# Performance work log

Hardware: AMD Instinct MI355X
Metric: run time of the kernel (lower is better)

## Reference

```python
import jax, jax.numpy as jnp
import numpy as np

NH = 4        # router attention heads
M1, M2 = 16, 16  # Fourier modes kept
N_FNO_LAYERS = 4
TOP_K = 2
TEMP = 1.0


def _ln(x, g, b):
    m = x.mean(-1, keepdims=True)
    v = ((x - m) ** 2).mean(-1, keepdims=True)
    return (x - m) / jnp.sqrt(v + 1e-5) * g + b


def _mha(s, wqkv, bqkv, wo, bo):
    B, S, D = s.shape
    dh = D // NH
    qkv = s @ wqkv + bqkv
    q, k, v = jnp.split(qkv, 3, axis=-1)
    rs = lambda t: t.reshape(B, S, NH, dh).transpose(0, 2, 1, 3)
    q, k, v = rs(q), rs(k), rs(v)
    a = jax.nn.softmax(jnp.einsum('bhqd,bhkd->bhqk', q, k) / np.sqrt(dh), axis=-1)
    o = jnp.einsum('bhqk,bhkd->bhqd', a, v).transpose(0, 2, 1, 3).reshape(B, S, D)
    return o @ wo + bo


def _spectral_conv(h, w1, w2):
    # h: (B, Ci, H, W); w1/w2: (Ci, Co, M1, M2, 2) real/imag pairs
    B, Ci, H, W = h.shape
    Co = w1.shape[1]
    ft = jnp.fft.rfft2(h, axes=(-2, -1))  # (B, Ci, H, W//2+1) complex
    w1c = w1[..., 0] + 1j * w1[..., 1]
    w2c = w2[..., 0] + 1j * w2[..., 1]
    lo = jnp.einsum('bixy,ioxy->boxy', ft[:, :, :M1, :M2], w1c)
    hi = jnp.einsum('bixy,ioxy->boxy', ft[:, :, -M1:, :M2], w2c)
    oft = jnp.zeros((B, Co, H, W // 2 + 1), dtype=ft.dtype)
    oft = oft.at[:, :, :M1, :M2].set(lo).at[:, :, -M1:, :M2].set(hi)
    return jnp.fft.irfft2(oft, s=(H, W), axes=(-2, -1))


def _fno(x, lw, lb, sw1, sw2, kw, kb, p1w, p1b, p2w, p2b):
    h = jnp.einsum('bchw,co->bohw', x, lw) + lb[None, :, None, None]
    for l in range(N_FNO_LAYERS):
        s = _spectral_conv(h, sw1[l], sw2[l])
        sk = jnp.einsum('bchw,co->bohw', h, kw[l]) + kb[l][None, :, None, None]
        h = s + sk
        if l < N_FNO_LAYERS - 1:
            h = jax.nn.gelu(h)
    h = jax.nn.gelu(jnp.einsum('bchw,co->bohw', h, p1w) + p1b[None, :, None, None])
    return jnp.einsum('bchw,co->bohw', h, p2w) + p2b[None, :, None, None]


def _router(x, enc_in_w, enc_in_b, attn_wqkv, attn_bqkv, attn_wo, attn_bo,
            ln1_g, ln1_b, ffn_w1, ffn_b1, ffn_w2, ffn_b2, ln2_g, ln2_b, fc_w, fc_b):
    ic = x[:, :, 0, :]                       # (B, C, W) initial condition
    s = ic.transpose(0, 2, 1) @ enc_in_w + enc_in_b  # (B, W, hd)
    for l in range(attn_wqkv.shape[0]):
        s = _ln(s + _mha(s, attn_wqkv[l], attn_bqkv[l], attn_wo[l], attn_bo[l]), ln1_g[l], ln1_b[l])
        f = jax.nn.relu(s @ ffn_w1[l] + ffn_b1[l]) @ ffn_w2[l] + ffn_b2[l]
        s = _ln(s + f, ln2_g[l], ln2_b[l])
    feat = s.max(axis=1)                     # global max-pool over sequence
    logits = feat @ fc_w + fc_b              # (B, E)
    vals, idx = jax.lax.top_k(logits, TOP_K)
    w = jax.nn.softmax(vals / TEMP, axis=-1)
    B = logits.shape[0]
    rw = jnp.zeros_like(logits).at[jnp.arange(B)[:, None], idx].set(w)
    return rw


def setup_inputs() -> dict:
    key = jax.random.key(0)
    ks = iter(jax.random.split(key, 40))
    B, C, H, W = 32, 1, 64, 64
    E, HC, HD, RL, FF, OC = 8, 64, 64, 2, 256, 1
    rn = lambda shp, sc: jax.random.normal(next(ks), shp, dtype=jnp.float32) * sc
    inp = {
        'x': rn((B, C, H, W), 1.0),
        'enc_in_w': rn((C, HD), 0.5), 'enc_in_b': jnp.zeros((HD,), jnp.float32),
        'attn_wqkv': rn((RL, HD, 3 * HD), 0.08), 'attn_bqkv': jnp.zeros((RL, 3 * HD), jnp.float32),
        'attn_wo': rn((RL, HD, HD), 0.08), 'attn_bo': jnp.zeros((RL, HD), jnp.float32),
        'ln1_g': jnp.ones((RL, HD), jnp.float32), 'ln1_b': jnp.zeros((RL, HD), jnp.float32),
        'ffn_w1': rn((RL, HD, FF), 0.08), 'ffn_b1': jnp.zeros((RL, FF), jnp.float32),
        'ffn_w2': rn((RL, FF, HD), 0.05), 'ffn_b2': jnp.zeros((RL, HD), jnp.float32),
        'ln2_g': jnp.ones((RL, HD), jnp.float32), 'ln2_b': jnp.zeros((RL, HD), jnp.float32),
        'fc_w': rn((HD, E), 0.1), 'fc_b': jnp.zeros((E,), jnp.float32),
        'lift_w': rn((E, C, HC), 0.3), 'lift_b': jnp.zeros((E, HC), jnp.float32),
        'spec_w1': rn((E, N_FNO_LAYERS, HC, HC, M1, M2, 2), 1.0 / HC),
        'spec_w2': rn((E, N_FNO_LAYERS, HC, HC, M1, M2, 2), 1.0 / HC),
        'skip_w': rn((E, N_FNO_LAYERS, HC, HC), 0.08), 'skip_b': jnp.zeros((E, N_FNO_LAYERS, HC), jnp.float32),
        'proj1_w': rn((E, HC, HC), 0.08), 'proj1_b': jnp.zeros((E, HC), jnp.float32),
        'proj2_w': rn((E, HC, OC), 0.08), 'proj2_b': jnp.zeros((E, OC), jnp.float32),
    }
    return inp


def reference(x, enc_in_w, enc_in_b, attn_wqkv, attn_bqkv, attn_wo, attn_bo,
              ln1_g, ln1_b, ffn_w1, ffn_b1, ffn_w2, ffn_b2, ln2_g, ln2_b, fc_w, fc_b,
              lift_w, lift_b, spec_w1, spec_w2, skip_w, skip_b,
              proj1_w, proj1_b, proj2_w, proj2_b):
    rw = _router(x, enc_in_w, enc_in_b, attn_wqkv, attn_bqkv, attn_wo, attn_bo,
                 ln1_g, ln1_b, ffn_w1, ffn_b1, ffn_w2, ffn_b2, ln2_g, ln2_b, fc_w, fc_b)
    E = rw.shape[1]
    out = jnp.zeros((x.shape[0], proj2_w.shape[2], x.shape[2], x.shape[3]), x.dtype)
    for e in range(E):
        # weight is 0 for non-selected experts, so dense weighted sum == masked dispatch
        y = _fno(x, lift_w[e], lift_b[e], spec_w1[e], spec_w2[e],
                 skip_w[e], skip_b[e], proj1_w[e], proj1_b[e], proj2_w[e], proj2_b[e])
        out = out + rw[:, e, None, None, None] * y
    return out
```

## Files before the change

kernel.cpp:

```cpp
#include <hip/hip_runtime.h>
#include <math.h>

#define TWOPI_F 6.283185307179586f
#define LD4(p) (*(const float4*)(p))

__device__ __forceinline__ float gelu_f(float v) {
    float u = 0.7978845608028654f * (v + 0.044715f * v * v * v);
    return 0.5f * v * (1.f + tanhf(u));
}

__global__ void init_tables_kernel(float* __restrict__ Wy, float* __restrict__ TWX,
                                   float* __restrict__ WY2) {
    int t = threadIdx.x;
    for (int i = t; i < 1024; i += 256) {
        int y = i >> 4, k = i & 15;
        int m = (k * y) & 63;
        float a = -TWOPI_F * (float)m / 64.f;
        Wy[y * 32 + 2 * k]     = cosf(a);
        Wy[y * 32 + 2 * k + 1] = sinf(a);
    }
    if (t < 64) {
        float a = -TWOPI_F * (float)t / 64.f;
        TWX[2 * t]           = cosf(a);
        TWX[2 * t + 1]       = sinf(a);
        TWX[128 + 2 * t]     = cosf(a);
        TWX[128 + 2 * t + 1] = -sinf(a);
    }
    for (int i = t; i < 1024; i += 256) {
        int y = i >> 4, k = i & 15;
        int m = (k * y) & 63;
        float a = TWOPI_F * (float)m / 64.f;
        float sc = (k == 0 ? 1.f : 2.f) / 4096.f;
        WY2[y * 32 + 2 * k]     = sc * cosf(a);
        WY2[y * 32 + 2 * k + 1] = sc * sinf(a);
    }
}

__global__ __launch_bounds__(512) void router_kernel(
    const float* __restrict__ x, const float* __restrict__ enc_w, const float* __restrict__ enc_b,
    const float* __restrict__ wqkv, const float* __restrict__ bqkv,
    const float* __restrict__ wo, const float* __restrict__ bo,
    const float* __restrict__ ln1g, const float* __restrict__ ln1b,
    const float* __restrict__ w1, const float* __restrict__ b1,
    const float* __restrict__ w2, const float* __restrict__ b2,
    const float* __restrict__ ln2g, const float* __restrict__ ln2b,
    const float* __restrict__ fcw, const float* __restrict__ fcb,
    float* __restrict__ rw)
{
    __shared__ float s[64][65];
    __shared__ float qk[64][193];
    __shared__ float sc[64][65];
    __shared__ float o64[64][65];
    __shared__ float feat[64];
    __shared__ float logits[8];
    int b = blockIdx.x, t = threadIdx.x;

    for (int i = t; i < 4096; i += 512) {
        int w_ = i >> 6, d = i & 63;
        s[w_][d] = x[b * 4096 + w_] * enc_w[d] + enc_b[d];
    }
    __syncthreads();

    for (int l = 0; l < 2; ++l) {
        {
            const float* Wq = wqkv + l * 64 * 192;
            const float* Bq = bqkv + l * 192;
            int c4 = t % 48, rg = t / 48;
            if (rg < 8) {
                const float* wcol = Wq + 4 * c4;
                float4 bq = LD4(Bq + 4 * c4);
                float4 acc[8];
#pragma unroll
                for (int i = 0; i < 8; ++i) acc[i] = bq;
                int r0 = rg * 8;
#pragma unroll 8
                for (int k = 0; k < 64; ++k) {
                    float4 wv = LD4(wcol + k * 192);
#pragma unroll
                    for (int i = 0; i < 8; ++i) {
                        float sv = s[r0 + i][k];
                        acc[i].x += sv * wv.x; acc[i].y += sv * wv.y;
                        acc[i].z += sv * wv.z; acc[i].w += sv * wv.w;
                    }
                }
#pragma unroll
                for (int i = 0; i < 8; ++i) {
                    qk[r0 + i][4 * c4]     = acc[i].x;
                    qk[r0 + i][4 * c4 + 1] = acc[i].y;
                    qk[r0 + i][4 * c4 + 2] = acc[i].z;
                    qk[r0 + i][4 * c4 + 3] = acc[i].w;
                }
            }
        }
        __syncthreads();
        for (int h = 0; h < 4; ++h) {
            for (int i = t; i < 4096; i += 512) {
                int q = i >> 6, kj = i & 63;
                float acc = 0.f;
#pragma unroll
                for (int d = 0; d < 16; ++d)
                    acc += qk[q][h * 16 + d] * qk[kj][64 + h * 16 + d];
                sc[q][kj] = acc * 0.25f;
            }
            __syncthreads();
            if (t < 64) {
                float m = -1e30f;
                for (int j = 0; j < 64; ++j) m = fmaxf(m, sc[t][j]);
                float sum = 0.f;
                for (int j = 0; j < 64; ++j) { float e2 = expf(sc[t][j] - m); sc[t][j] = e2; sum += e2; }
                float inv = 1.f / sum;
                for (int j = 0; j < 64; ++j) sc[t][j] *= inv;
            }
            __syncthreads();
            for (int i = t; i < 1024; i += 512) {
                int q = i >> 4, d = i & 15;
                float acc = 0.f;
#pragma unroll 8
                for (int j = 0; j < 64; ++j) acc += sc[q][j] * qk[j][128 + h * 16 + d];
                o64[q][h * 16 + d] = acc;
            }
            __syncthreads();
        }
        {
            const float* Wo = wo + l * 4096;
            const float* Bo = bo + l * 64;
            int c4 = t & 15, rg = t >> 4;
            const float* wcol = Wo + 4 * c4;
            float4 acc0 = LD4(Bo + 4 * c4), acc1 = acc0;
            int r0 = rg * 2;
#pragma unroll 8
            for (int k = 0; k < 64; ++k) {
                float4 wv = LD4(wcol + k * 64);
                float h0 = o64[r0][k], h1 = o64[r0 + 1][k];
                acc0.x += h0 * wv.x; acc0.y += h0 * wv.y;
                acc0.z += h0 * wv.z; acc0.w += h0 * wv.w;
                acc1.x += h1 * wv.x; acc1.y += h1 * wv.y;
                acc1.z += h1 * wv.z; acc1.w += h1 * wv.w;
            }
            sc[r0][4 * c4]     = s[r0][4 * c4]     + acc0.x;
            sc[r0][4 * c4 + 1] = s[r0][4 * c4 + 1] + acc0.y;
            sc[r0][4 * c4 + 2] = s[r0][4 * c4 + 2] + acc0.z;
            sc[r0][4 * c4 + 3] = s[r0][4 * c4 + 3] + acc0.w;
            sc[r0 + 1][4 * c4]     = s[r0 + 1][4 * c4]     + acc1.x;
            sc[r0 + 1][4 * c4 + 1] = s[r0 + 1][4 * c4 + 1] + acc1.y;
            sc[r0 + 1][4 * c4 + 2] = s[r0 + 1][4 * c4 + 2] + acc1.z;
            sc[r0 + 1][4 * c4 + 3] = s[r0 + 1][4 * c4 + 3] + acc1.w;
        }
        __syncthreads();
        if (t < 64) {
            float m = 0.f;
            for (int j = 0; j < 64; ++j) m += sc[t][j];
            m *= (1.f / 64.f);
            float v = 0.f;
            for (int j = 0; j < 64; ++j) { float d = sc[t][j] - m; v += d * d; }
            v *= (1.f / 64.f);
            float inv = rsqrtf(v + 1e-5f);
            for (int j = 0; j < 64; ++j)
                s[t][j] = (sc[t][j] - m) * inv * ln1g[l * 64 + j] + ln1b[l * 64 + j];
        }
        __syncthreads();
        {
            const float* W1 = w1 + l * 64 * 256;
            const float* B1 = b1 + l * 256;
            int c4 = t & 63, rg = t >> 6;
            const float* wcol = W1 + 4 * c4;
            float4 b1v = LD4(B1 + 4 * c4);
            float4 acc[8];
#pragma unroll
            for (int i = 0; i < 8; ++i) acc[i] = b1v;
            int r0 = rg * 8;
#pragma unroll 4
            for (int k = 0; k < 64; ++k) {
                float4 wv = LD4(wcol + k * 256);
#pragma unroll
                for (int i = 0; i < 8; ++i) {
                    float sv = s[r0 + i][k];
                    acc[i].x += sv * wv.x; acc[i].y += sv * wv.y;
                    acc[i].z += sv * wv.z; acc[i].w += sv * wv.w;
                }
            }
#pragma unroll
            for (int i = 0; i < 8; ++i) {
                float a0 = fmaxf(acc[i].x, 0.f), a1 = fmaxf(acc[i].y, 0.f);
                float a2 = fmaxf(acc[i].z, 0.f), a3 = fmaxf(acc[i].w, 0.f);
                if (c4 < 48) {
                    qk[r0 + i][4 * c4] = a0; qk[r0 + i][4 * c4 + 1] = a1;
                    qk[r0 + i][4 * c4 + 2] = a2; qk[r0 + i][4 * c4 + 3] = a3;
                } else {
                    int c = 4 * c4 - 192;
                    o64[r0 + i][c] = a0; o64[r0 + i][c + 1] = a1;
                    o64[r0 + i][c + 2] = a2; o64[r0 + i][c + 3] = a3;
                }
            }
        }
        __syncthreads();
        {
            const float* W2 = w2 + l * 256 * 64;
            const float* B2 = b2 + l * 64;
            int c4 = t & 15, rg = t >> 4;
            const float* wcol = W2 + 4 * c4;
            float4 acc0 = LD4(B2 + 4 * c4), acc1 = acc0;
            int r0 = rg * 2;
#pragma unroll 8
            for (int k = 0; k < 192; ++k) {
                float4 wv = LD4(wcol + k * 64);
                float h0 = qk[r0][k], h1 = qk[r0 + 1][k];
                acc0.x += h0 * wv.x; acc0.y += h0 * wv.y;
                acc0.z += h0 * wv.z; acc0.w += h0 * wv.w;
                acc1.x += h1 * wv.x; acc1.y += h1 * wv.y;
                acc1.z += h1 * wv.z; acc1.w += h1 * wv.w;
            }
#pragma unroll 8
            for (int k = 192; k < 256; ++k) {
                float4 wv = LD4(wcol + k * 64);
                float h0 = o64[r0][k - 192], h1 = o64[r0 + 1][k - 192];
                acc0.x += h0 * wv.x; acc0.y += h0 * wv.y;
                acc0.z += h0 * wv.z; acc0.w += h0 * wv.w;
                acc1.x += h1 * wv.x; acc1.y += h1 * wv.y;
                acc1.z += h1 * wv.z; acc1.w += h1 * wv.w;
            }
            sc[r0][4 * c4]     = s[r0][4 * c4]     + acc0.x;
            sc[r0][4 * c4 + 1] = s[r0][4 * c4 + 1] + acc0.y;
            sc[r0][4 * c4 + 2] = s[r0][4 * c4 + 2] + acc0.z;
            sc[r0][4 * c4 + 3] = s[r0][4 * c4 + 3] + acc0.w;
            sc[r0 + 1][4 * c4]     = s[r0 + 1][4 * c4]     + acc1.x;
            sc[r0 + 1][4 * c4 + 1] = s[r0 + 1][4 * c4 + 1] + acc1.y;
            sc[r0 + 1][4 * c4 + 2] = s[r0 + 1][4 * c4 + 2] + acc1.z;
            sc[r0 + 1][4 * c4 + 3] = s[r0 + 1][4 * c4 + 3] + acc1.w;
        }
        __syncthreads();
        if (t < 64) {
            float m = 0.f;
            for (int j = 0; j < 64; ++j) m += sc[t][j];
            m *= (1.f / 64.f);
            float v = 0.f;
            for (int j = 0; j < 64; ++j) { float d = sc[t][j] - m; v += d * d; }
            v *= (1.f / 64.f);
            float inv = rsqrtf(v + 1e-5f);
            for (int j = 0; j < 64; ++j)
                s[t][j] = (sc[t][j] - m) * inv * ln2g[l * 64 + j] + ln2b[l * 64 + j];
        }
        __syncthreads();
    }
    if (t < 64) {
        float m = -1e30f;
        for (int r = 0; r < 64; ++r) m = fmaxf(m, s[r][t]);
        feat[t] = m;
    }
    __syncthreads();
    if (t < 8) {
        float acc = fcb[t];
        for (int k = 0; k < 64; ++k) acc += feat[k] * fcw[k * 8 + t];
        logits[t] = acc;
    }
    __syncthreads();
    if (t == 0) {
        int i0 = 0;
        for (int j = 1; j < 8; ++j) if (logits[j] > logits[i0]) i0 = j;
        int i1 = -1;
        for (int j = 0; j < 8; ++j) {
            if (j == i0) continue;
            if (i1 < 0 || logits[j] > logits[i1]) i1 = j;
        }
        float e1 = expf(logits[i1] - logits[i0]);
        float w0 = 1.f / (1.f + e1);
        float w1v = e1 / (1.f + e1);
        for (int j = 0; j < 8; ++j) rw[b * 8 + j] = 0.f;
        rw[b * 8 + i0] = w0;
        rw[b * 8 + i1] = w1v;
    }
}

__global__ void build_pairs_kernel(const float* __restrict__ rw, int* __restrict__ pair_b,
                                   int* __restrict__ pair_e, float* __restrict__ pair_w,
                                   int* __restrict__ estart, int* __restrict__ chunk_e,
                                   int* __restrict__ chunk_p0, int* __restrict__ chunk_np) {
    __shared__ float r[256];
    __shared__ int cnt[8], off[9];
    int t = threadIdx.x;
    for (int i = t; i < 256; i += 64) r[i] = rw[i];
    if (t < 64) { pair_b[t] = 0; pair_e[t] = 0; pair_w[t] = 0.f; }
    __syncthreads();
    if (t < 8) {
        int c = 0;
        for (int b = 0; b < 32; ++b) if (r[b * 8 + t] != 0.f) ++c;
        cnt[t] = c;
    }
    __syncthreads();
    if (t == 0) {
        int a = 0;
        for (int e = 0; e < 8; ++e) { off[e] = a; a += cnt[e]; }
        off[8] = a;
        for (int e = 0; e <= 8; ++e) estart[e] = off[e];
        int nc = 0;
        for (int e = 0; e < 8; ++e) {
            for (int s = off[e]; s < off[e + 1]; s += 8) {
                int np = off[e + 1] - s; if (np > 8) np = 8;
                chunk_e[nc] = e; chunk_p0[nc] = s; chunk_np[nc] = np; ++nc;
            }
        }
        for (int c = nc; c < 16; ++c) { chunk_e[c] = 0; chunk_p0[c] = 0; chunk_np[c] = 0; }
    }
    __syncthreads();
    if (t < 8) {
        int n = off[t];
        for (int b = 0; b < 32; ++b) {
            float w = r[b * 8 + t];
            if (w != 0.f) { pair_b[n] = b; pair_e[n] = t; pair_w[n] = w; ++n; }
        }
    }
}

__global__ __launch_bounds__(256) void lift_kernel(const float* __restrict__ x,
    const float* __restrict__ lw, const float* __restrict__ lb,
    const int* __restrict__ pair_b, const int* __restrict__ pair_e, float* __restrict__ hA) {
    int p = blockIdx.x, tile = blockIdx.y, t = threadIdx.x;
    int b = pair_b[p], e = pair_e[p];
    float* h = hA + (size_t)p * 262144;
    const float* xb = x + (size_t)b * 4096;
    for (int i = tile * 16384 + t; i < (tile + 1) * 16384; i += 256) {
        int co = i >> 12, xy = i & 4095;
        h[i] = xb[xy] * lw[e * 64 + co] + lb[e * 64 + co];
    }
}

__global__ __launch_bounds__(256) void fwdft_kernel(const float* __restrict__ h,
    const float* __restrict__ Wy, const float* __restrict__ TWX, float* __restrict__ F) {
    __shared__ float ht[64][68];
    __shared__ float gt[64][36];
    __shared__ float wy[2048];
    __shared__ float tw64[128];
    int bid = blockIdx.x;
    int t = threadIdx.x;
    const float* src = h + (size_t)bid * 4096;
    for (int i = t; i < 1024; i += 256) {
        float4 v = *(const float4*)(src + i * 4);
        int x = (i * 4) >> 6, y = (i * 4) & 63;
        *(float4*)(&ht[x][y]) = v;
    }
    for (int i = t; i < 512; i += 256) *(float4*)(&wy[i * 4]) = *(const float4*)(Wy + i * 4);
    if (t < 32) *(float4*)(&tw64[t * 4]) = LD4(TWX + t * 4);
    __syncthreads();
    {
        int xx = t >> 2, kq = t & 3;
        float gr0 = 0.f, gi0 = 0.f, gr1 = 0.f, gi1 = 0.f;
        float gr2 = 0.f, gi2 = 0.f, gr3 = 0.f, gi3 = 0.f;
#pragma unroll 4
        for (int y = 0; y < 64; ++y) {
            float hv = ht[xx][y];
            float4 w0 = *(const float4*)(&wy[y * 32 + kq * 8]);
            float4 w1 = *(const float4*)(&wy[y * 32 + kq * 8 + 4]);
            gr0 += hv * w0.x; gi0 += hv * w0.y;
            gr1 += hv * w0.z; gi1 += hv * w0.w;
            gr2 += hv * w1.x; gi2 += hv * w1.y;
            gr3 += hv * w1.z; gi3 += hv * w1.w;
        }
        *(float4*)(&gt[xx][kq * 8])     = make_float4(gr0, gi0, gr1, gi1);
        *(float4*)(&gt[xx][kq * 8 + 4]) = make_float4(gr2, gi2, gr3, gi3);
    }
    __syncthreads();
    {
        int kxm = t & 31, kyq = t >> 5;
        int kx = kxm < 16 ? kxm : kxm + 32;
        float ar0 = 0.f, ai0 = 0.f, ar1 = 0.f, ai1 = 0.f;
        int idx = 0;
#pragma unroll 4
        for (int xx = 0; xx < 64; ++xx) {
            float c_ = tw64[2 * idx], s_ = tw64[2 * idx + 1];
            float4 g = *(const float4*)(&gt[xx][kyq * 4]);
            ar0 += g.x * c_ - g.y * s_;  ai0 += g.x * s_ + g.y * c_;
            ar1 += g.z * c_ - g.w * s_;  ai1 += g.z * s_ + g.w * c_;
            idx = (idx + kx) & 63;
        }
        float* fb = F + (size_t)bid * 1024 + kxm * 32 + kyq * 4;
        *(float4*)(fb) = make_float4(ar0, ai0, ar1, ai1);
    }
}

__global__ __launch_bounds__(256) void spectral_kernel(
    const float* __restrict__ F, float* __restrict__ FoA, float* __restrict__ FoB,
    const float* __restrict__ w1, const float* __restrict__ w2,
    const int* __restrict__ chunk_e, const int* __restrict__ chunk_p0,
    const int* __restrict__ chunk_np, int l)
{
    int c = blockIdx.x;
    int np = chunk_np[c];
    if (np == 0) return;
    int e = chunk_e[c], p0 = chunk_p0[c];
    int z = blockIdx.z;
    int wsel = z & 1, cih = (z >> 1) & 1, mq = z >> 2;
    int t = threadIdx.x;
    int co = blockIdx.y * 4 + (t >> 6);
    int lane = t & 63;
    int moff = mq * 256 + lane * 4;

    const float* wbase = (wsel == 0 ? w1 : w2) + (size_t)(e * 4 + l) * 2097152;
    const float* Wc  = wbase + (size_t)(cih * 32) * 32768 + (size_t)co * 512 + moff;
    const float* Fc0 = F + (size_t)p0 * 65536 + (size_t)(cih * 32) * 1024 + wsel * 512 + moff;
    float* Fob = (cih ? FoB : FoA) + (size_t)p0 * 65536 + (size_t)co * 1024 + wsel * 512 + moff;

    float4 acc[8];
#pragma unroll
    for (int p = 0; p < 8; ++p) acc[p] = make_float4(0.f, 0.f, 0.f, 0.f);
    const float* Wp = Wc;
    const float* Fp = Fc0;
    for (int ci = 0; ci < 32; ++ci) {
        float4 wv = LD4(Wp);
#pragma unroll
        for (int p = 0; p < 8; ++p) {
            float4 fv = LD4(Fp + (size_t)p * 65536);
            acc[p].x += fv.x * wv.x - fv.y * wv.y;
            acc[p].y += fv.x * wv.y + fv.y * wv.x;
            acc[p].z += fv.z * wv.z - fv.w * wv.w;
            acc[p].w += fv.z * wv.w + fv.w * wv.z;
        }
        Wp += 32768;
        Fp += 1024;
    }
#pragma unroll
    for (int p = 0; p < 8; ++p) {
        if (p < np)
            *(float4*)(Fob + (size_t)p * 65536) = acc[p];
    }
}

__global__ __launch_bounds__(256) void conv1x1_kernel(
    const float* __restrict__ src, float* __restrict__ dst,
    const float* __restrict__ Wall, const float* __restrict__ Ball,
    const int* __restrict__ pair_e, int wmul, int wadd, int do_gelu)
{
    __shared__ float ws[64][68];
    __shared__ float bs[64];
    int p = blockIdx.x, tile = blockIdx.y, t = threadIdx.x;
    int e = pair_e[p];
    int widx = e * wmul + wadd;
    const float* W = Wall + (size_t)widx * 4096;
    for (int i = t; i < 1024; i += 256) {
        float4 v = LD4(W + i * 4);
        int ci = (i * 4) >> 6, co = (i * 4) & 63;
        *(float4*)(&ws[ci][co]) = v;
    }
    if (t < 64) bs[t] = Ball[widx * 64 + t];
    __syncthreads();

    int xy4 = t & 63, cog = t >> 6;
    const float* sb = src + (size_t)p * 262144 + tile * 256 + xy4 * 4;
    float4 acc[16];
#pragma unroll
    for (int j = 0; j < 16; ++j) {
        float bv = bs[cog * 16 + j];
        acc[j] = make_float4(bv, bv, bv, bv);
    }
    for (int ci = 0; ci < 64; ++ci) {
        float4 sv = LD4(sb + (size_t)ci * 4096);
        float4 w0 = *(const float4*)(&ws[ci][cog * 16]);
        float4 w1 = *(const float4*)(&ws[ci][cog * 16 + 4]);
        float4 w2 = *(const float4*)(&ws[ci][cog * 16 + 8]);
        float4 w3 = *(const float4*)(&ws[ci][cog * 16 + 12]);
        float wr[16] = {w0.x, w0.y, w0.z, w0.w, w1.x, w1.y, w1.z, w1.w,
                        w2.x, w2.y, w2.z, w2.w, w3.x, w3.y, w3.z, w3.w};
#pragma unroll
        for (int j = 0; j < 16; ++j) {
            float w = wr[j];
            acc[j].x += sv.x * w; acc[j].y += sv.y * w;
            acc[j].z += sv.z * w; acc[j].w += sv.w * w;
        }
    }
    float* d = dst + (size_t)p * 262144 + (size_t)(cog * 16) * 4096 + tile * 256 + xy4 * 4;
#pragma unroll
    for (int j = 0; j < 16; ++j) {
        float4 v = acc[j];
        if (do_gelu) {
            v.x = gelu_f(v.x); v.y = gelu_f(v.y);
            v.z = gelu_f(v.z); v.w = gelu_f(v.w);
        }
        *(float4*)(d + (size_t)j * 4096) = v;
    }
}

__global__ __launch_bounds__(256) void projfused_kernel(
    const float* __restrict__ src, const float* __restrict__ p1w,
    const float* __restrict__ p1b, const float* __restrict__ p2w,
    const float* __restrict__ p2b, const int* __restrict__ pair_b,
    const int* __restrict__ pair_e, const float* __restrict__ pw,
    float* __restrict__ out)
{
    __shared__ float ws[64][68];
    __shared__ float bs[64];
    __shared__ float w2s[64];
    __shared__ float4 red[4][64];
    int p = blockIdx.x, tile = blockIdx.y, t = threadIdx.x;
    int e = pair_e[p];
    const float* W = p1w + (size_t)e * 4096;
    for (int i = t; i < 1024; i += 256) {
        float4 v = LD4(W + i * 4);
        int ci = (i * 4) >> 6, co = (i * 4) & 63;
        *(float4*)(&ws[ci][co]) = v;
    }
    if (t < 64) { bs[t] = p1b[e * 64 + t]; w2s[t] = p2w[e * 64 + t]; }
    __syncthreads();

    int xy4 = t & 63, cog = t >> 6;
    const float* sb = src + (size_t)p * 262144 + tile * 256 + xy4 * 4;
    float4 acc[16];
#pragma unroll
    for (int j = 0; j < 16; ++j) {
        float bv = bs[cog * 16 + j];
        acc[j] = make_float4(bv, bv, bv, bv);
    }
    for (int ci = 0; ci < 64; ++ci) {
        float4 sv = LD4(sb + (size_t)ci * 4096);
        float4 w0 = *(const float4*)(&ws[ci][cog * 16]);
        float4 w1 = *(const float4*)(&ws[ci][cog * 16 + 4]);
        float4 w2 = *(const float4*)(&ws[ci][cog * 16 + 8]);
        float4 w3 = *(const float4*)(&ws[ci][cog * 16 + 12]);
        float wr[16] = {w0.x, w0.y, w0.z, w0.w, w1.x, w1.y, w1.z, w1.w,
                        w2.x, w2.y, w2.z, w2.w, w3.x, w3.y, w3.z, w3.w};
#pragma unroll
        for (int j = 0; j < 16; ++j) {
            float w = wr[j];
            acc[j].x += sv.x * w; acc[j].y += sv.y * w;
            acc[j].z += sv.z * w; acc[j].w += sv.w * w;
        }
    }
    float4 part = make_float4(0.f, 0.f, 0.f, 0.f);
#pragma unroll
    for (int j = 0; j < 16; ++j) {
        float w = w2s[cog * 16 + j];
        part.x += gelu_f(acc[j].x) * w;
        part.y += gelu_f(acc[j].y) * w;
        part.z += gelu_f(acc[j].z) * w;
        part.w += gelu_f(acc[j].w) * w;
    }
    red[cog][xy4] = part;
    __syncthreads();
    if (t < 64) {
        float4 s0 = red[0][t], s1 = red[1][t], s2 = red[2][t], s3 = red[3][t];
        float wgt = pw[p];
        float b2 = p2b[e];
        int b = pair_b[p];
        float* ob = out + (size_t)b * 4096 + tile * 256 + t * 4;
        atomicAdd(ob,     wgt * (s0.x + s1.x + s2.x + s3.x + b2));
        atomicAdd(ob + 1, wgt * (s0.y + s1.y + s2.y + s3.y + b2));
        atomicAdd(ob + 2, wgt * (s0.z + s1.z + s2.z + s3.z + b2));
        atomicAdd(ob + 3, wgt * (s0.w + s1.w + s2.w + s3.w + b2));
    }
}

__global__ __launch_bounds__(256) void inv_kernel(
    const float* __restrict__ FoA, const float* __restrict__ FoB,
    const float* __restrict__ WY2, const float* __restrict__ TWX,
    float* __restrict__ dst_h, int do_gelu)
{
    __shared__ float wy2[2048];
    __shared__ float twl[128];
    __shared__ float fo_s[1024];
    __shared__ float tT[64][36];
    __shared__ float ot[64][66];
    int t = threadIdx.x;
    for (int i = t; i < 512; i += 256) *(float4*)(&wy2[i * 4]) = *(const float4*)(WY2 + i * 4);
    if (t < 32) *(float4*)(&twl[t * 4]) = LD4(TWX + 128 + t * 4);
    int wid = blockIdx.x;
    int p = wid >> 6, co = wid & 63;
    const float* fA = FoA + (size_t)p * 65536 + (size_t)co * 1024;
    const float* fB = FoB + (size_t)p * 65536 + (size_t)co * 1024;
    {
        float4 a = LD4(fA + t * 4);
        float4 b = LD4(fB + t * 4);
        *(float4*)(&fo_s[t * 4]) = make_float4(a.x + b.x, a.y + b.y, a.z + b.z, a.w + b.w);
    }
    __syncthreads();
    {
        int xx = t & 63, kq = t >> 6;
        float Tr0 = 0.f, Ti0 = 0.f, Tr1 = 0.f, Ti1 = 0.f;
        float Tr2 = 0.f, Ti2 = 0.f, Tr3 = 0.f, Ti3 = 0.f;
#pragma unroll 4
        for (int kxm = 0; kxm < 32; ++kxm) {
            int kx = kxm < 16 ? kxm : kxm + 32;
            int idx = (kx * xx) & 63;
            float c_ = twl[2 * idx], s_ = twl[2 * idx + 1];
            float4 f0 = *(const float4*)(&fo_s[kxm * 32 + kq * 8]);
            float4 f1 = *(const float4*)(&fo_s[kxm * 32 + kq * 8 + 4]);
            Tr0 += f0.x * c_ - f0.y * s_;  Ti0 += f0.x * s_ + f0.y * c_;
            Tr1 += f0.z * c_ - f0.w * s_;  Ti1 += f0.z * s_ + f0.w * c_;
            Tr2 += f1.x * c_ - f1.y * s_;  Ti2 += f1.x * s_ + f1.y * c_;
            Tr3 += f1.z * c_ - f1.w * s_;  Ti3 += f1.z * s_ + f1.w * c_;
        }
        *(float4*)(&tT[xx][kq * 8])     = make_float4(Tr0, Ti0, Tr1, Ti1);
        *(float4*)(&tT[xx][kq * 8 + 4]) = make_float4(Tr2, Ti2, Tr3, Ti3);
    }
    __syncthreads();
    {
        int xx = t & 63, yq = t >> 6;
        float Trr[16], Tii[16];
#pragma unroll
        for (int q = 0; q < 8; ++q) {
            float4 v = *(const float4*)(&tT[xx][q * 4]);
            Trr[q * 2] = v.x; Tii[q * 2] = v.y;
            Trr[q * 2 + 1] = v.z; Tii[q * 2 + 1] = v.w;
        }
        for (int j = 0; j < 16; ++j) {
            int y = yq * 16 + j;
            const float* wr = &wy2[y * 32];
            float acc = 0.f;
#pragma unroll
            for (int k = 0; k < 16; ++k)
                acc += Trr[k] * wr[2 * k] - Tii[k] * wr[2 * k + 1];
            ot[xx][y] = acc;
        }
    }
    __syncthreads();
    {
        float* base = dst_h + (size_t)p * 262144 + (size_t)co * 4096;
        for (int r = 0; r < 16; ++r) {
            int gidx = r * 256 + t;
            int xx = gidx >> 6, y = gidx & 63;
            float v = base[gidx] + ot[xx][y];
            if (do_gelu) v = gelu_f(v);
            base[gidx] = v;
        }
    }
}

extern "C" void kernel_launch(void* const* d_in, const int* in_sizes, int n_in,
                              void* d_out, int out_size, void* d_ws, size_t ws_size,
                              hipStream_t stream) {
    const float* x    = (const float*)d_in[0];
    const float* encw = (const float*)d_in[1];
    const float* encb = (const float*)d_in[2];
    const float* wqkv = (const float*)d_in[3];
    const float* bqkv = (const float*)d_in[4];
    const float* wo   = (const float*)d_in[5];
    const float* bo   = (const float*)d_in[6];
    const float* ln1g = (const float*)d_in[7];
    const float* ln1b = (const float*)d_in[8];
    const float* fw1  = (const float*)d_in[9];
    const float* fb1  = (const float*)d_in[10];
    const float* fw2  = (const float*)d_in[11];
    const float* fb2  = (const float*)d_in[12];
    const float* ln2g = (const float*)d_in[13];
    const float* ln2b = (const float*)d_in[14];
    const float* fcw  = (const float*)d_in[15];
    const float* fcb  = (const float*)d_in[16];
    const float* lw   = (const float*)d_in[17];
    const float* lb   = (const float*)d_in[18];
    const float* sw1  = (const float*)d_in[19];
    const float* sw2  = (const float*)d_in[20];
    const float* skw  = (const float*)d_in[21];
    const float* skb  = (const float*)d_in[22];
    const float* p1w  = (const float*)d_in[23];
    const float* p1b  = (const float*)d_in[24];
    const float* p2w  = (const float*)d_in[25];
    const float* p2b  = (const float*)d_in[26];
    float* out = (float*)d_out;

    float* wsf    = (float*)d_ws;
    float* rw     = wsf;
    float* pair_w = wsf + 256;
    int*   ipart  = (int*)(wsf + 320);
    int* pair_b   = ipart;
    int* pair_e   = ipart + 64;
    int* estart   = ipart + 128;
    int* chunk_e  = ipart + 137;
    int* chunk_p0 = ipart + 153;
    int* chunk_np = ipart + 169;
    float* Wy  = wsf + 512;
    float* TWX = wsf + 2560;
    float* WY2 = wsf + 6656;
    float* hA  = wsf + 16384;
    float* hB  = hA + (size_t)64 * 262144;
    float* F   = hB + (size_t)64 * 262144;
    float* FoA = F + (size_t)64 * 65536;
    float* FoB = FoA + (size_t)64 * 65536;
    size_t need = (16384 + 2ull * 64 * 262144 + 64ull * 65536 + 64ull * 131072) * 4;
    if (ws_size < need) return;

    hipMemsetAsync(d_out, 0, (size_t)out_size * sizeof(float), stream);
    init_tables_kernel<<<1, 256, 0, stream>>>(Wy, TWX, WY2);
    router_kernel<<<32, 512, 0, stream>>>(x, encw, encb, wqkv, bqkv, wo, bo, ln1g, ln1b,
                                          fw1, fb1, fw2, fb2, ln2g, ln2b, fcw, fcb, rw);
    build_pairs_kernel<<<1, 64, 0, stream>>>(rw, pair_b, pair_e, pair_w, estart,
                                             chunk_e, chunk_p0, chunk_np);
    lift_kernel<<<dim3(64, 16), 256, 0, stream>>>(x, lw, lb, pair_b, pair_e, hA);
    for (int l = 0; l < 4; ++l) {
        float* cur = (l & 1) ? hB : hA;
        float* nxt = (l & 1) ? hA : hB;
        fwdft_kernel<<<4096, 256, 0, stream>>>(cur, Wy, TWX, F);
        spectral_kernel<<<dim3(16, 16, 8), 256, 0, stream>>>(F, FoA, FoB, sw1, sw2,
                                                             chunk_e, chunk_p0, chunk_np, l);
        conv1x1_kernel<<<dim3(64, 16), 256, 0, stream>>>(cur, nxt, skw, skb, pair_e, 4, l, 0);
        inv_kernel<<<4096, 256, 0, stream>>>(FoA, FoB, WY2, TWX, nxt, (l < 3) ? 1 : 0);
    }
    projfused_kernel<<<dim3(64, 16), 256, 0, stream>>>(hA, p1w, p1b, p2w, p2b,
                                                       pair_b, pair_e, pair_w, out);
}
```

Before: 1.322 ms.

## Fuse lift into first-layer DFT and skip conv; batch router attention heads

Removes the separate lift kernel and its 64x64x4096 activation write. The lift is now recomputed inline from x in a new forward-DFT kernel and a new 1x1 skip-conv kernel for layer 0. This saves one full write and read pass of the hA buffer per pair. Separately, the router computes all four attention heads' scores, softmax and outputs in single passes with a larger per-head score buffer, cutting the number of barriers. The cost is more shared memory in the router and some redundant lift arithmetic per channel.

After: 1.300 ms. No clear change (-1.6%).

```diff
diff --git a/kernel.cpp b/kernel.cpp
--- a/kernel.cpp
+++ b/kernel.cpp
@@ -49,7 +49,7 @@
 {
     __shared__ float s[64][65];
     __shared__ float qk[64][193];
-    __shared__ float sc[64][65];
+    __shared__ float scH[4][64][65];
     __shared__ float o64[64][65];
     __shared__ float feat[64];
     __shared__ float logits[8];
@@ -93,34 +93,34 @@
             }
         }
         __syncthreads();
-        for (int h = 0; h < 4; ++h) {
-            for (int i = t; i < 4096; i += 512) {
-                int q = i >> 6, kj = i & 63;
-                float acc = 0.f;
-#pragma unroll
-                for (int d = 0; d < 16; ++d)
-                    acc += qk[q][h * 16 + d] * qk[kj][64 + h * 16 + d];
-                sc[q][kj] = acc * 0.25f;
-            }
-            __syncthreads();
-            if (t < 64) {
-                float m = -1e30f;
-                for (int j = 0; j < 64; ++j) m = fmaxf(m, sc[t][j]);
-                float sum = 0.f;
-                for (int j = 0; j < 64; ++j) { float e2 = expf(sc[t][j] - m); sc[t][j] = e2; sum += e2; }
-                float inv = 1.f / sum;
-                for (int j = 0; j < 64; ++j) sc[t][j] *= inv;
-            }
-            __syncthreads();
-            for (int i = t; i < 1024; i += 512) {
-                int q = i >> 4, d = i & 15;
-                float acc = 0.f;
+        for (int i = t; i < 16384; i += 512) {
+            int h = i >> 12, q = (i >> 6) & 63, kj = i & 63;
+            float acc = 0.f;
+#pragma unroll
+            for (int d = 0; d < 16; ++d)
+                acc += qk[q][h * 16 + d] * qk[kj][64 + h * 16 + d];
+            scH[h][q][kj] = acc * 0.25f;
+        }
+        __syncthreads();
+        if (t < 256) {
+            int h = t >> 6, q = t & 63;
+            float* row = scH[h][q];
+            float m = -1e30f;
+            for (int j = 0; j < 64; ++j) m = fmaxf(m, row[j]);
+            float sum = 0.f;
+            for (int j = 0; j < 64; ++j) { float e2 = expf(row[j] - m); row[j] = e2; sum += e2; }
+            float inv = 1.f / sum;
+            for (int j = 0; j < 64; ++j) row[j] *= inv;
+        }
+        __syncthreads();
+        for (int i = t; i < 4096; i += 512) {
+            int q = i >> 6, d = i & 63, h = d >> 4;
+            float acc = 0.f;
 #pragma unroll 8
-                for (int j = 0; j < 64; ++j) acc += sc[q][j] * qk[j][128 + h * 16 + d];
-                o64[q][h * 16 + d] = acc;
-            }
-            __syncthreads();
-        }
+            for (int j = 0; j < 64; ++j) acc += scH[h][q][j] * qk[j][128 + d];
+            o64[q][d] = acc;
+        }
+        __syncthreads();
         {
             const float* Wo = wo + l * 4096;
             const float* Bo = bo + l * 64;
@@ -137,26 +137,26 @@
                 acc1.x += h1 * wv.x; acc1.y += h1 * wv.y;
                 acc1.z += h1 * wv.z; acc1.w += h1 * wv.w;
             }
-            sc[r0][4 * c4]     = s[r0][4 * c4]     + acc0.x;
-            sc[r0][4 * c4 + 1] = s[r0][4 * c4 + 1] + acc0.y;
-            sc[r0][4 * c4 + 2] = s[r0][4 * c4 + 2] + acc0.z;
-            sc[r0][4 * c4 + 3] = s[r0][4 * c4 + 3] + acc0.w;
-            sc[r0 + 1][4 * c4]     = s[r0 + 1][4 * c4]     + acc1.x;
-            sc[r0 + 1][4 * c4 + 1] = s[r0 + 1][4 * c4 + 1] + acc1.y;
-            sc[r0 + 1][4 * c4 + 2] = s[r0 + 1][4 * c4 + 2] + acc1.z;
-            sc[r0 + 1][4 * c4 + 3] = s[r0 + 1][4 * c4 + 3] + acc1.w;
+            scH[0][r0][4 * c4]     = s[r0][4 * c4]     + acc0.x;
+            scH[0][r0][4 * c4 + 1] = s[r0][4 * c4 + 1] + acc0.y;
+            scH[0][r0][4 * c4 + 2] = s[r0][4 * c4 + 2] + acc0.z;
+            scH[0][r0][4 * c4 + 3] = s[r0][4 * c4 + 3] + acc0.w;
+            scH[0][r0 + 1][4 * c4]     = s[r0 + 1][4 * c4]     + acc1.x;
+            scH[0][r0 + 1][4 * c4 + 1] = s[r0 + 1][4 * c4 + 1] + acc1.y;
+            scH[0][r0 + 1][4 * c4 + 2] = s[r0 + 1][4 * c4 + 2] + acc1.z;
+            scH[0][r0 + 1][4 * c4 + 3] = s[r0 + 1][4 * c4 + 3] + acc1.w;
         }
         __syncthreads();
         if (t < 64) {
             float m = 0.f;
-            for (int j = 0; j < 64; ++j) m += sc[t][j];
+            for (int j = 0; j < 64; ++j) m += scH[0][t][j];
             m *= (1.f / 64.f);
             float v = 0.f;
-            for (int j = 0; j < 64; ++j) { float d = sc[t][j] - m; v += d * d; }
+            for (int j = 0; j < 64; ++j) { float d = scH[0][t][j] - m; v += d * d; }
             v *= (1.f / 64.f);
             float inv = rsqrtf(v + 1e-5f);
             for (int j = 0; j < 64; ++j)
-                s[t][j] = (sc[t][j] - m) * inv * ln1g[l * 64 + j] + ln1b[l * 64 + j];
+                s[t][j] = (scH[0][t][j] - m) * inv * ln1g[l * 64 + j] + ln1b[l * 64 + j];
         }
         __syncthreads();
         {
@@ -219,26 +219,26 @@
                 acc1.x += h1 * wv.x; acc1.y += h1 * wv.y;
                 acc1.z += h1 * wv.z; acc1.w += h1 * wv.w;
             }
-            sc[r0][4 * c4]     = s[r0][4 * c4]     + acc0.x;
-            sc[r0][4 * c4 + 1] = s[r0][4 * c4 + 1] + acc0.y;
-            sc[r0][4 * c4 + 2] = s[r0][4 * c4 + 2] + acc0.z;
-            sc[r0][4 * c4 + 3] = s[r0][4 * c4 + 3] + acc0.w;
-            sc[r0 + 1][4 * c4]     = s[r0 + 1][4 * c4]     + acc1.x;
-            sc[r0 + 1][4 * c4 + 1] = s[r0 + 1][4 * c4 + 1] + acc1.y;
-            sc[r0 + 1][4 * c4 + 2] = s[r0 + 1][4 * c4 + 2] + acc1.z;
-            sc[r0 + 1][4 * c4 + 3] = s[r0 + 1][4 * c4 + 3] + acc1.w;
+            scH[0][r0][4 * c4]     = s[r0][4 * c4]     + acc0.x;
+            scH[0][r0][4 * c4 + 1] = s[r0][4 * c4 + 1] + acc0.y;
+            scH[0][r0][4 * c4 + 2] = s[r0][4 * c4 + 2] + acc0.z;
+            scH[0][r0][4 * c4 + 3] = s[r0][4 * c4 + 3] + acc0.w;
+            scH[0][r0 + 1][4 * c4]     = s[r0 + 1][4 * c4]     + acc1.x;
+            scH[0][r0 + 1][4 * c4 + 1] = s[r0 + 1][4 * c4 + 1] + acc1.y;
+            scH[0][r0 + 1][4 * c4 + 2] = s[r0 + 1][4 * c4 + 2] + acc1.z;
+            scH[0][r0 + 1][4 * c4 + 3] = s[r0 + 1][4 * c4 + 3] + acc1.w;
         }
         __syncthreads();
         if (t < 64) {
             float m = 0.f;
-            for (int j = 0; j < 64; ++j) m += sc[t][j];
+            for (int j = 0; j < 64; ++j) m += scH[0][t][j];
             m *= (1.f / 64.f);
             float v = 0.f;
-            for (int j = 0; j < 64; ++j) { float d = sc[t][j] - m; v += d * d; }
+            for (int j = 0; j < 64; ++j) { float d = scH[0][t][j] - m; v += d * d; }
             v *= (1.f / 64.f);
             float inv = rsqrtf(v + 1e-5f);
             for (int j = 0; j < 64; ++j)
-                s[t][j] = (sc[t][j] - m) * inv * ln2g[l * 64 + j] + ln2b[l * 64 + j];
+                s[t][j] = (scH[0][t][j] - m) * inv * ln2g[l * 64 + j] + ln2b[l * 64 + j];
         }
         __syncthreads();
     }
@@ -308,19 +308,6 @@
             float w = r[b * 8 + t];
             if (w != 0.f) { pair_b[n] = b; pair_e[n] = t; pair_w[n] = w; ++n; }
         }
-    }
-}
-
-__global__ __launch_bounds__(256) void lift_kernel(const float* __restrict__ x,
-    const float* __restrict__ lw, const float* __restrict__ lb,
-    const int* __restrict__ pair_b, const int* __restrict__ pair_e, float* __restrict__ hA) {
-    int p = blockIdx.x, tile = blockIdx.y, t = threadIdx.x;
-    int b = pair_b[p], e = pair_e[p];
-    float* h = hA + (size_t)p * 262144;
-    const float* xb = x + (size_t)b * 4096;
-    for (int i = tile * 16384 + t; i < (tile + 1) * 16384; i += 256) {
-        int co = i >> 12, xy = i & 4095;
-        h[i] = xb[xy] * lw[e * 64 + co] + lb[e * 64 + co];
     }
 }
 
@@ -337,6 +324,67 @@
         float4 v = *(const float4*)(src + i * 4);
         int x = (i * 4) >> 6, y = (i * 4) & 63;
         *(float4*)(&ht[x][y]) = v;
+    }
+    for (int i = t; i < 512; i += 256) *(float4*)(&wy[i * 4]) = *(const float4*)(Wy + i * 4);
+    if (t < 32) *(float4*)(&tw64[t * 4]) = LD4(TWX + t * 4);
+    __syncthreads();
+    {
+        int xx = t >> 2, kq = t & 3;
+        float gr0 = 0.f, gi0 = 0.f, gr1 = 0.f, gi1 = 0.f;
+        float gr2 = 0.f, gi2 = 0.f, gr3 = 0.f, gi3 = 0.f;
+#pragma unroll 4
+        for (int y = 0; y < 64; ++y) {
+            float hv = ht[xx][y];
+            float4 w0 = *(const float4*)(&wy[y * 32 + kq * 8]);
+            float4 w1 = *(const float4*)(&wy[y * 32 + kq * 8 + 4]);
+            gr0 += hv * w0.x; gi0 += hv * w0.y;
+            gr1 += hv * w0.z; gi1 += hv * w0.w;
+            gr2 += hv * w1.x; gi2 += hv * w1.y;
+            gr3 += hv * w1.z; gi3 += hv * w1.w;
+        }
+        *(float4*)(&gt[xx][kq * 8])     = make_float4(gr0, gi0, gr1, gi1);
+        *(float4*)(&gt[xx][kq * 8 + 4]) = make_float4(gr2, gi2, gr3, gi3);
+    }
+    __syncthreads();
+    {
+        int kxm = t & 31, kyq = t >> 5;
+        int kx = kxm < 16 ? kxm : kxm + 32;
+        float ar0 = 0.f, ai0 = 0.f, ar1 = 0.f, ai1 = 0.f;
+        int idx = 0;
+#pragma unroll 4
+        for (int xx = 0; xx < 64; ++xx) {
+            float c_ = tw64[2 * idx], s_ = tw64[2 * idx + 1];
+            float4 g = *(const float4*)(&gt[xx][kyq * 4]);
+            ar0 += g.x * c_ - g.y * s_;  ai0 += g.x * s_ + g.y * c_;
+            ar1 += g.z * c_ - g.w * s_;  ai1 += g.z * s_ + g.w * c_;
+            idx = (idx + kx) & 63;
+        }
+        float* fb = F + (size_t)bid * 1024 + kxm * 32 + kyq * 4;
+        *(float4*)(fb) = make_float4(ar0, ai0, ar1, ai1);
+    }
+}
+
+__global__ __launch_bounds__(256) void fwdft_x_kernel(const float* __restrict__ x,
+    const float* __restrict__ lw, const float* __restrict__ lb,
+    const int* __restrict__ pair_b, const int* __restrict__ pair_e,
+    const float* __restrict__ Wy, const float* __restrict__ TWX, float* __restrict__ F) {
+    __shared__ float ht[64][68];
+    __shared__ float gt[64][36];
+    __shared__ float wy[2048];
+    __shared__ float tw64[128];
+    int bid = blockIdx.x;
+    int t = threadIdx.x;
+    int p = bid >> 6, ci = bid & 63;
+    int e = pair_e[p], b = pair_b[p];
+    float lwv = lw[e * 64 + ci];
+    float lbv = lb[e * 64 + ci];
+    const float* src = x + (size_t)b * 4096;
+    for (int i = t; i < 1024; i += 256) {
+        float4 v = *(const float4*)(src + i * 4);
+        v.x = v.x * lwv + lbv; v.y = v.y * lwv + lbv;
+        v.z = v.z * lwv + lbv; v.w = v.w * lwv + lbv;
+        int xx = (i * 4) >> 6, y = (i * 4) & 63;
+        *(float4*)(&ht[xx][y]) = v;
     }
     for (int i = t; i < 512; i += 256) *(float4*)(&wy[i * 4]) = *(const float4*)(Wy + i * 4);
     if (t < 32) *(float4*)(&tw64[t * 4]) = LD4(TWX + t * 4);
@@ -476,6 +524,63 @@
         }
         *(float4*)(d + (size_t)j * 4096) = v;
     }
+}
+
+__global__ __launch_bounds__(256) void conv1x1_x_kernel(
+    const float* __restrict__ x, float* __restrict__ dst,
+    const float* __restrict__ Wall, const float* __restrict__ Ball,
+    const float* __restrict__ lw, const float* __restrict__ lb,
+    const int* __restrict__ pair_b, const int* __restrict__ pair_e)
+{
+    __shared__ float ws[64][68];
+    __shared__ float bs[64];
+    __shared__ float lws[64];
+    __shared__ float lbs[64];
+    int p = blockIdx.x, tile = blockIdx.y, t = threadIdx.x;
+    int e = pair_e[p], b = pair_b[p];
+    int widx = e * 4;
+    const float* W = Wall + (size_t)widx * 4096;
+    for (int i = t; i < 1024; i += 256) {
+        float4 v = LD4(W + i * 4);
+        int ci = (i * 4) >> 6, co = (i * 4) & 63;
+        *(float4*)(&ws[ci][co]) = v;
+    }
+    if (t < 64) {
+        bs[t]  = Ball[widx * 64 + t];
+        lws[t] = lw[e * 64 + t];
+        lbs[t] = lb[e * 64 + t];
+    }
+    __syncthreads();
+
+    int xy4 = t & 63, cog = t >> 6;
+    float4 xv = LD4(x + (size_t)b * 4096 + tile * 256 + xy4 * 4);
+    float4 acc[16];
+#pragma unroll
+    for (int j = 0; j < 16; ++j) {
+        float bv = bs[cog * 16 + j];
+        acc[j] = make_float4(bv, bv, bv, bv);
+    }
+    for (int ci = 0; ci < 64; ++ci) {
+        float lwv = lws[ci], lbv = lbs[ci];
+        float4 sv = make_float4(xv.x * lwv + lbv, xv.y * lwv + lbv,
+                                xv.z * lwv + lbv, xv.w * lwv + lbv);
+        float4 w0 = *(const float4*)(&ws[ci][cog * 16]);
+        float4 w1 = *(const float4*)(&ws[ci][cog * 16 + 4]);
+        float4 w2 = *(const float4*)(&ws[ci][cog * 16 + 8]);
+        float4 w3 = *(const float4*)(&ws[ci][cog * 16 + 12]);
+        float wr[16] = {w0.x, w0.y, w0.z, w0.w, w1.x, w1.y, w1.z, w1.w,
+                        w2.x, w2.y, w2.z, w2.w, w3.x, w3.y, w3.z, w3.w};
+#pragma unroll
+        for (int j = 0; j < 16; ++j) {
+            float w = wr[j];
+            acc[j].x += sv.x * w; acc[j].y += sv.y * w;
+            acc[j].z += sv.z * w; acc[j].w += sv.w * w;
+        }
+    }
+    float* d = dst + (size_t)p * 262144 + (size_t)(cog * 16) * 4096 + tile * 256 + xy4 * 4;
+#pragma unroll
+    for (int j = 0; j < 16; ++j)
+        *(float4*)(d + (size_t)j * 4096) = acc[j];
 }
 
 __global__ __launch_bounds__(256) void projfused_kernel(
@@ -681,14 +786,22 @@
                                           fw1, fb1, fw2, fb2, ln2g, ln2b, fcw, fcb, rw);
     build_pairs_kernel<<<1, 64, 0, stream>>>(rw, pair_b, pair_e, pair_w, estart,
                                              chunk_e, chunk_p0, chunk_np);
-    lift_kernel<<<dim3(64, 16), 256, 0, stream>>>(x, lw, lb, pair_b, pair_e, hA);
     for (int l = 0; l < 4; ++l) {
         float* cur = (l & 1) ? hB : hA;
         float* nxt = (l & 1) ? hA : hB;
-        fwdft_kernel<<<4096, 256, 0, stream>>>(cur, Wy, TWX, F);
+        if (l == 0) {
+            fwdft_x_kernel<<<4096, 256, 0, stream>>>(x, lw, lb, pair_b, pair_e, Wy, TWX, F);
+        } else {
+            fwdft_kernel<<<4096, 256, 0, stream>>>(cur, Wy, TWX, F);
+        }
         spectral_kernel<<<dim3(16, 16, 8), 256, 0, stream>>>(F, FoA, FoB, sw1, sw2,
                                                              chunk_e, chunk_p0, chunk_np, l);
-        conv1x1_kernel<<<dim3(64, 16), 256, 0, stream>>>(cur, nxt, skw, skb, pair_e, 4, l, 0);
+        if (l == 0) {
+            conv1x1_x_kernel<<<dim3(64, 16), 256, 0, stream>>>(x, nxt, skw, skb,
+                                                               lw, lb, pair_b, pair_e);
+        } else {
+            conv1x1_kernel<<<dim3(64, 16), 256, 0, stream>>>(cur, nxt, skw, skb, pair_e, 4, l, 0);
+        }
         inv_kernel<<<4096, 256, 0, stream>>>(FoA, FoB, WY2, TWX, nxt, (l < 3) ? 1 : 0);
     }
     projfused_kernel<<<dim3(64, 16), 256, 0, stream>>>(hA, p1w, p1b, p2w, p2b,
```
